# Kernel optimization log

Measured on AMD Instinct MI355X. Metric: run time of the kernel, lower is better.

## Reference

```python
import jax, jax.numpy as jnp
import numpy as np

# Circuit structure constants (match init_kwargs)
N_NODES = 32768        # number of sum nodes in this layer
N_CHILD = 65536        # number of child nodes
NNZ = 1048576          # number of sparse weight entries (avg fan-in 32)
BATCH = 128


def setup_inputs() -> dict:
    key = jax.random.key(0)
    k1, k2, k3, k4 = jax.random.split(key, 4)
    # child log-likelihoods per sample (output of child layers)
    child_ll = jax.random.normal(k1, (BATCH, N_CHILD), dtype=jnp.float32)
    # sparse log-weights of the BCOO weight matrix [N_NODES, N_CHILD]
    log_w = jax.random.normal(k2, (NNZ,), dtype=jnp.float32)
    rows = jnp.sort(jax.random.randint(k3, (NNZ,), 0, N_NODES)).astype(jnp.int64)
    cols = jax.random.randint(k4, (NNZ,), 0, N_CHILD).astype(jnp.int64)
    return {"child_ll": child_ll, "log_w": log_w, "rows": rows, "cols": cols}


def reference(child_ll, log_w, rows, cols):
    """Faithful jax translation of SumLayer.log_likelihood_of_nodes.

    Original: per sample, exponentiate BCOO log-weights and child
    log-likelihoods, sparse matvec (weights @ exp(child_ll)), then
    log(result) - log_normalization_constants, where the normalization
    constants are log(row-sums of exp(log_weights)).
    """
    w = jnp.exp(log_w)  # [NNZ]
    # log normalization constants: log of row-sums of exp(log_weights)
    log_z = jnp.log(jax.ops.segment_sum(w, rows, num_segments=N_NODES))  # [N_NODES]

    def per_sample(ll):  # ll: [N_CHILD]
        p = jnp.exp(ll)
        contrib = w * p[cols]                                   # gather + weight [NNZ]
        return jax.ops.segment_sum(contrib, rows, num_segments=N_NODES)  # [N_NODES]

    s = jax.vmap(per_sample)(child_ll)  # [BATCH, N_NODES]
    return jnp.log(s) - log_z
```

## Files before the change

kernel.cpp:

```cpp
#include <hip/hip_runtime.h>
#include <math.h>

#define BATCH     128
#define N_NODES   32768
#define N_CHILD   65536
#define NNZ_TOTAL 1048576

typedef __attribute__((ext_vector_type(2))) float fx2;

__global__ __launch_bounds__(256) void exp_transpose_fp8_kernel(
    const float* __restrict__ child_ll, unsigned char* __restrict__ ex8,
    float* __restrict__ winv) {
    __shared__ float tile[64][BATCH + 1];
    __shared__ float sc[64];
    const int c0 = blockIdx.x * 64;
    const int t  = threadIdx.x;

    {
        const int cl = t & 63;
        const int b0 = t >> 6;
#pragma unroll
        for (int j = 0; j < BATCH / 4; ++j) {
            const int b = b0 + j * 4;
            tile[cl][b] = expf(child_ll[(size_t)b * N_CHILD + c0 + cl]);
        }
    }
    __syncthreads();

    if (t < 64) {
        float m = tile[t][0];
#pragma unroll 4
        for (int b = 1; b < BATCH; ++b) m = fmaxf(m, tile[t][b]);
        const int k = 7 - ilogbf(m);
        sc[t] = ldexpf(1.f, k);
        winv[c0 + t] = ldexpf(1.f, -k);
    }
    __syncthreads();

    {
        const int sub = t & 7;
        const int b0  = sub * 16;
#pragma unroll
        for (int p = 0; p < 2; ++p) {
            const int c = (t >> 3) + p * 32;
            const float s = sc[c];
            uint4 o;
            unsigned* ow = (unsigned*)&o;
#pragma unroll
            for (int q = 0; q < 4; ++q) {
                unsigned v = 0;
                v = __builtin_amdgcn_cvt_pk_fp8_f32(
                        tile[c][b0 + q * 4 + 0] * s, tile[c][b0 + q * 4 + 1] * s, v, false);
                v = __builtin_amdgcn_cvt_pk_fp8_f32(
                        tile[c][b0 + q * 4 + 2] * s, tile[c][b0 + q * 4 + 3] * s, v, true);
                ow[q] = v;
            }
            *(uint4*)&ex8[(size_t)(c0 + c) * 128 + (unsigned)b0] = o;
        }
    }
}

__global__ __launch_bounds__(256) void prep_kernel(
    const float* __restrict__ log_w, const int* __restrict__ cols,
    const float* __restrict__ winv, const int* __restrict__ rows,
    float* __restrict__ wfold, int* __restrict__ row_start) {
    const int bid = blockIdx.x;
    const int t   = threadIdx.x;
    if (bid < 1024) {
        const int i = (bid * 256 + t) * 4;
        const float4 lw = *(const float4*)&log_w[i];
        const int4   cc = *(const int4*)&cols[i];
        float4 o;
        o.x = expf(lw.x) * winv[cc.x];
        o.y = expf(lw.y) * winv[cc.y];
        o.z = expf(lw.z) * winv[cc.z];
        o.w = expf(lw.w) * winv[cc.w];
        *(float4*)&wfold[i] = o;
    } else {
        const int r = (bid - 1024) * 256 + t;
        if (r > N_NODES) return;
        if (r == N_NODES) { row_start[r] = NNZ_TOTAL; return; }
        int lo = 0, hi = NNZ_TOTAL;
        while (lo < hi) {
            const int mid = (lo + hi) >> 1;
            if (rows[mid] < r) lo = mid + 1; else hi = mid;
        }
        row_start[r] = lo;
    }
}

__global__ __launch_bounds__(256, 4) void sum_rows_kernel(
    const unsigned char* __restrict__ ex8, const float* __restrict__ wfold,
    const float* __restrict__ log_w, const int* __restrict__ cols,
    const int* __restrict__ row_start, float* __restrict__ out) {
    const int wave = threadIdx.x >> 6;
    const int lane = threadIdx.x & 63;
    const int bid  = blockIdx.x;
    const int rb   = (bid & 7) * (N_NODES / 4 / 8) + (bid >> 3);
    const int r    = rb * 4 + wave;

    const int start = row_start[r];
    const int end   = row_start[r + 1];
    const int  slot = lane >> 3;
    const unsigned sub = (unsigned)lane & 7u;
    const unsigned boff = sub * 16u;

    float acc[16];
#pragma unroll
    for (int k = 0; k < 16; ++k) acc[k] = 0.f;
    float wlane = 0.f;

    for (int base = start; base < end; base += 64) {
        const int  idx   = base + lane;
        const bool valid = idx < end;
        const int   c  = __builtin_nontemporal_load(&cols[valid ? idx : start]);
        const float wf = valid ? __builtin_nontemporal_load(&wfold[idx]) : 0.f;
        wlane += valid ? expf(__builtin_nontemporal_load(&log_w[idx])) : 0.f;
        const int seg = end - base;

        int   ct[8];
        float wt[8];
        uint4 g[8];

#pragma unroll
        for (int t8 = 0; t8 < 8; ++t8) {
            if (t8 * 8 < seg) {
                const int pa = (t8 * 8 + slot) * 4;
                ct[t8] = __builtin_amdgcn_ds_bpermute(pa, c);
                wt[t8] = __uint_as_float(__builtin_amdgcn_ds_bpermute(
                    pa, __float_as_uint(wf)));
            }
        }
#pragma unroll
        for (int t8 = 0; t8 < 8; ++t8) {
            if (t8 * 8 < seg)
                g[t8] = *(const uint4*)(ex8 +
                        ((size_t)(unsigned)ct[t8] << 7) + boff);
        }
#pragma unroll
        for (int t8 = 0; t8 < 8; ++t8) {
            if (t8 * 8 < seg) {
                const float wtv = wt[t8];
                const unsigned* gu = (const unsigned*)&g[t8];
#pragma unroll
                for (int q = 0; q < 4; ++q) {
                    const fx2 lo = __builtin_amdgcn_cvt_pk_f32_fp8((int)gu[q], false);
                    const fx2 hi = __builtin_amdgcn_cvt_pk_f32_fp8((int)gu[q], true);
                    acc[q * 4 + 0] = fmaf(wtv, lo.x, acc[q * 4 + 0]);
                    acc[q * 4 + 1] = fmaf(wtv, lo.y, acc[q * 4 + 1]);
                    acc[q * 4 + 2] = fmaf(wtv, hi.x, acc[q * 4 + 2]);
                    acc[q * 4 + 3] = fmaf(wtv, hi.y, acc[q * 4 + 3]);
                }
            }
        }
    }

#pragma unroll
    for (int k = 0; k < 16; ++k) {
        acc[k] += __shfl_xor(acc[k], 8, 64);
        acc[k] += __shfl_xor(acc[k], 16, 64);
        acc[k] += __shfl_xor(acc[k], 32, 64);
    }
    float wsum = wlane;
#pragma unroll
    for (int m = 1; m < 64; m <<= 1) wsum += __shfl_xor(wsum, m, 64);
    const float logz = logf(wsum);

    if (lane < 8) {
        const int b0 = lane * 16;
#pragma unroll
        for (int k = 0; k < 16; ++k)
            out[(size_t)(b0 + k) * N_NODES + r] = logf(acc[k]) - logz;
    }
}

extern "C" void kernel_launch(void* const* d_in, const int* in_sizes, int n_in,
                              void* d_out, int out_size, void* d_ws, size_t ws_size,
                              hipStream_t stream) {
    const float* child_ll = (const float*)d_in[0];
    const float* log_w    = (const float*)d_in[1];
    const int*   rows     = (const int*)d_in[2];
    const int*   cols     = (const int*)d_in[3];
    float*       out      = (float*)d_out;

    unsigned char* ex8    = (unsigned char*)d_ws;
    float* winv      = (float*)((char*)d_ws + (size_t)N_CHILD * 128);
    float* wfold     = (float*)((char*)winv + (size_t)N_CHILD * 4);
    int*   row_start = (int*)((char*)wfold + (size_t)NNZ_TOTAL * 4);

    exp_transpose_fp8_kernel<<<N_CHILD / 64, 256, 0, stream>>>(child_ll, ex8, winv);
    prep_kernel<<<1024 + 129, 256, 0, stream>>>(log_w, cols, winv, rows,
                                                wfold, row_start);
    sum_rows_kernel<<<N_NODES / 4, 256, 0, stream>>>(ex8, wfold, log_w, cols,
                                                     row_start, out);
}
```

Baseline: 70.88 us.

## Restructure exp/fp8 pack, move log-normalizer to prep, LDS reduction in row kernel

The exp/transpose kernel now keeps child values in registers, picks the scale from the raw max via floor(x*log2e), folds the scale into exp2, and stages packed fp8 bytes through LDS. The prep kernel computes the per-row log normalizer with 16-lane groups next to the binary search, so the row kernel no longer reads log_w or runs exp on it. The row kernel loads cols and weights directly per slot instead of using bpermute, and replaces shuffle reductions with an LDS reduction so all 64 lanes write outputs. This trades redundant per-slot global loads and an extra barrier for less ALU work and wider stores.

```diff
diff --git a/kernel.cpp b/kernel.cpp
--- a/kernel.cpp
+++ b/kernel.cpp
@@ -5,65 +5,73 @@
 #define N_NODES   32768
 #define N_CHILD   65536
 #define NNZ_TOTAL 1048576
+#define LOG2E     1.44269504f
 
 typedef __attribute__((ext_vector_type(2))) float fx2;
 
-__global__ __launch_bounds__(256) void exp_transpose_fp8_kernel(
+__global__ __launch_bounds__(256) void exp8_kernel(
     const float* __restrict__ child_ll, unsigned char* __restrict__ ex8,
     float* __restrict__ winv) {
-    __shared__ float tile[64][BATCH + 1];
-    __shared__ float sc[64];
     const int c0 = blockIdx.x * 64;
     const int t  = threadIdx.x;
-
-    {
-        const int cl = t & 63;
-        const int b0 = t >> 6;
-#pragma unroll
-        for (int j = 0; j < BATCH / 4; ++j) {
-            const int b = b0 + j * 4;
-            tile[cl][b] = expf(child_ll[(size_t)b * N_CHILD + c0 + cl]);
-        }
-    }
-    __syncthreads();
-
+    const int cl = t & 63;
+    const int q  = t >> 6;
+
+    float v[32];
+    float m = -3.4e38f;
+    const float* bp = child_ll + (size_t)(q * 32) * N_CHILD + c0 + cl;
+#pragma unroll
+    for (int j = 0; j < 32; ++j) {
+        v[j] = bp[(size_t)j * N_CHILD];
+        m = fmaxf(m, v[j]);
+    }
+
+    __shared__ float smx[4][64];
+    __shared__ float skf[64];
+    smx[q][cl] = m;
+    __syncthreads();
     if (t < 64) {
-        float m = tile[t][0];
-#pragma unroll 4
-        for (int b = 1; b < BATCH; ++b) m = fmaxf(m, tile[t][b]);
-        const int k = 7 - ilogbf(m);
-        sc[t] = ldexpf(1.f, k);
-        winv[c0 + t] = ldexpf(1.f, -k);
-    }
-    __syncthreads();
-
-    {
-        const int sub = t & 7;
-        const int b0  = sub * 16;
-#pragma unroll
-        for (int p = 0; p < 2; ++p) {
-            const int c = (t >> 3) + p * 32;
-            const float s = sc[c];
-            uint4 o;
-            unsigned* ow = (unsigned*)&o;
-#pragma unroll
-            for (int q = 0; q < 4; ++q) {
-                unsigned v = 0;
-                v = __builtin_amdgcn_cvt_pk_fp8_f32(
-                        tile[c][b0 + q * 4 + 0] * s, tile[c][b0 + q * 4 + 1] * s, v, false);
-                v = __builtin_amdgcn_cvt_pk_fp8_f32(
-                        tile[c][b0 + q * 4 + 2] * s, tile[c][b0 + q * 4 + 3] * s, v, true);
-                ow[q] = v;
-            }
-            *(uint4*)&ex8[(size_t)(c0 + c) * 128 + (unsigned)b0] = o;
-        }
+        const float mm = fmaxf(fmaxf(smx[0][t], smx[1][t]),
+                               fmaxf(smx[2][t], smx[3][t]));
+        const int ks = 7 - (int)floorf(mm * LOG2E);
+        skf[t] = (float)ks;
+        winv[c0 + t] = exp2f((float)(-ks));
+    }
+    __syncthreads();
+    const float kf = skf[cl];
+
+    unsigned ow[8];
+#pragma unroll
+    for (int p = 0; p < 8; ++p) {
+        const float a0 = exp2f(fmaf(v[4 * p + 0], LOG2E, kf));
+        const float a1 = exp2f(fmaf(v[4 * p + 1], LOG2E, kf));
+        const float a2 = exp2f(fmaf(v[4 * p + 2], LOG2E, kf));
+        const float a3 = exp2f(fmaf(v[4 * p + 3], LOG2E, kf));
+        unsigned u = 0;
+        u = __builtin_amdgcn_cvt_pk_fp8_f32(a0, a1, u, false);
+        u = __builtin_amdgcn_cvt_pk_fp8_f32(a2, a3, u, true);
+        ow[p] = u;
+    }
+
+    __shared__ unsigned char sby[64 * 144];
+    *(uint4*)&sby[cl * 144 + q * 32]      = *(uint4*)&ow[0];
+    *(uint4*)&sby[cl * 144 + q * 32 + 16] = *(uint4*)&ow[4];
+    __syncthreads();
+
+    const int sub = t & 7, cc = t >> 3;
+#pragma unroll
+    for (int p = 0; p < 2; ++p) {
+        const int c = cc + p * 32;
+        *(uint4*)&ex8[(size_t)(c0 + c) * 128 + sub * 16] =
+            *(const uint4*)&sby[c * 144 + sub * 16];
     }
 }
 
 __global__ __launch_bounds__(256) void prep_kernel(
     const float* __restrict__ log_w, const int* __restrict__ cols,
     const float* __restrict__ winv, const int* __restrict__ rows,
-    float* __restrict__ wfold, int* __restrict__ row_start) {
+    float* __restrict__ wfold, int* __restrict__ row_start,
+    float* __restrict__ logzv) {
     const int bid = blockIdx.x;
     const int t   = threadIdx.x;
     if (bid < 1024) {
@@ -76,23 +84,37 @@
         o.z = expf(lw.z) * winv[cc.z];
         o.w = expf(lw.w) * winv[cc.w];
         *(float4*)&wfold[i] = o;
+        if (bid == 0 && t == 0) row_start[N_NODES] = NNZ_TOTAL;
     } else {
-        const int r = (bid - 1024) * 256 + t;
-        if (r > N_NODES) return;
-        if (r == N_NODES) { row_start[r] = NNZ_TOTAL; return; }
+        const int wave = t >> 6, lane = t & 63;
+        const int grp = lane >> 4, j = lane & 15;
+        const int r = (bid - 1024) * 16 + wave * 4 + grp;
         int lo = 0, hi = NNZ_TOTAL;
         while (lo < hi) {
             const int mid = (lo + hi) >> 1;
             if (rows[mid] < r) lo = mid + 1; else hi = mid;
         }
-        row_start[r] = lo;
+        const int s = lo;
+        int lo2 = s, hi2 = NNZ_TOTAL;
+        while (lo2 < hi2) {
+            const int mid = (lo2 + hi2) >> 1;
+            if (rows[mid] < r + 1) lo2 = mid + 1; else hi2 = mid;
+        }
+        const int e = lo2;
+        float sum = 0.f;
+        for (int i = s + j; i < e; i += 16) sum += expf(log_w[i]);
+        sum += __shfl_xor(sum, 1, 64);
+        sum += __shfl_xor(sum, 2, 64);
+        sum += __shfl_xor(sum, 4, 64);
+        sum += __shfl_xor(sum, 8, 64);
+        if (j == 0) { row_start[r] = s; logzv[r] = logf(sum); }
     }
 }
 
 __global__ __launch_bounds__(256, 4) void sum_rows_kernel(
     const unsigned char* __restrict__ ex8, const float* __restrict__ wfold,
-    const float* __restrict__ log_w, const int* __restrict__ cols,
-    const int* __restrict__ row_start, float* __restrict__ out) {
+    const int* __restrict__ cols, const int* __restrict__ row_start,
+    const float* __restrict__ logzv, float* __restrict__ out) {
     const int wave = threadIdx.x >> 6;
     const int lane = threadIdx.x & 63;
     const int bid  = blockIdx.x;
@@ -101,23 +123,16 @@
 
     const int start = row_start[r];
     const int end   = row_start[r + 1];
-    const int  slot = lane >> 3;
-    const unsigned sub = (unsigned)lane & 7u;
-    const unsigned boff = sub * 16u;
+    const int slot  = lane >> 3;
+    const int sub   = lane & 7;
+    const unsigned boff = (unsigned)sub * 16u;
 
     float acc[16];
 #pragma unroll
     for (int k = 0; k < 16; ++k) acc[k] = 0.f;
-    float wlane = 0.f;
 
     for (int base = start; base < end; base += 64) {
-        const int  idx   = base + lane;
-        const bool valid = idx < end;
-        const int   c  = __builtin_nontemporal_load(&cols[valid ? idx : start]);
-        const float wf = valid ? __builtin_nontemporal_load(&wfold[idx]) : 0.f;
-        wlane += valid ? expf(__builtin_nontemporal_load(&log_w[idx])) : 0.f;
         const int seg = end - base;
-
         int   ct[8];
         float wt[8];
         uint4 g[8];
@@ -125,10 +140,9 @@
 #pragma unroll
         for (int t8 = 0; t8 < 8; ++t8) {
             if (t8 * 8 < seg) {
-                const int pa = (t8 * 8 + slot) * 4;
-                ct[t8] = __builtin_amdgcn_ds_bpermute(pa, c);
-                wt[t8] = __uint_as_float(__builtin_amdgcn_ds_bpermute(
-                    pa, __float_as_uint(wf)));
+                const int i = base + t8 * 8 + slot;
+                ct[t8] = cols[min(i, NNZ_TOTAL - 1)];
+                wt[t8] = (i < end) ? wfold[i] : 0.f;
             }
         }
 #pragma unroll
@@ -155,23 +169,26 @@
         }
     }
 
-#pragma unroll
-    for (int k = 0; k < 16; ++k) {
-        acc[k] += __shfl_xor(acc[k], 8, 64);
-        acc[k] += __shfl_xor(acc[k], 16, 64);
-        acc[k] += __shfl_xor(acc[k], 32, 64);
-    }
-    float wsum = wlane;
-#pragma unroll
-    for (int m = 1; m < 64; m <<= 1) wsum += __shfl_xor(wsum, m, 64);
-    const float logz = logf(wsum);
-
-    if (lane < 8) {
-        const int b0 = lane * 16;
-#pragma unroll
-        for (int k = 0; k < 16; ++k)
-            out[(size_t)(b0 + k) * N_NODES + r] = logf(acc[k]) - logz;
-    }
+    __shared__ float red[4][8][132];
+#pragma unroll
+    for (int u = 0; u < 4; ++u) {
+        const float4 vv = {acc[4 * u], acc[4 * u + 1],
+                           acc[4 * u + 2], acc[4 * u + 3]};
+        *(float4*)&red[wave][slot][sub * 16 + 4 * u] = vv;
+    }
+    __syncthreads();
+
+    const int b0 = lane * 2;
+    float s0 = 0.f, s1 = 0.f;
+#pragma unroll
+    for (int sl = 0; sl < 8; ++sl) {
+        const float2 p = *(const float2*)&red[wave][sl][b0];
+        s0 += p.x;
+        s1 += p.y;
+    }
+    const float lz = logzv[r];
+    out[(size_t)b0 * N_NODES + r]       = logf(s0) - lz;
+    out[(size_t)(b0 + 1) * N_NODES + r] = logf(s1) - lz;
 }
 
 extern "C" void kernel_launch(void* const* d_in, const int* in_sizes, int n_in,
@@ -183,14 +200,15 @@
     const int*   cols     = (const int*)d_in[3];
     float*       out      = (float*)d_out;
 
-    unsigned char* ex8    = (unsigned char*)d_ws;
+    unsigned char* ex8 = (unsigned char*)d_ws;
     float* winv      = (float*)((char*)d_ws + (size_t)N_CHILD * 128);
     float* wfold     = (float*)((char*)winv + (size_t)N_CHILD * 4);
     int*   row_start = (int*)((char*)wfold + (size_t)NNZ_TOTAL * 4);
-
-    exp_transpose_fp8_kernel<<<N_CHILD / 64, 256, 0, stream>>>(child_ll, ex8, winv);
-    prep_kernel<<<1024 + 129, 256, 0, stream>>>(log_w, cols, winv, rows,
-                                                wfold, row_start);
-    sum_rows_kernel<<<N_NODES / 4, 256, 0, stream>>>(ex8, wfold, log_w, cols,
-                                                     row_start, out);
-}
+    float* logzv     = (float*)((char*)row_start + (size_t)(N_NODES + 1) * 4);
+
+    exp8_kernel<<<N_CHILD / 64, 256, 0, stream>>>(child_ll, ex8, winv);
+    prep_kernel<<<3072, 256, 0, stream>>>(log_w, cols, winv, rows,
+                                          wfold, row_start, logzv);
+    sum_rows_kernel<<<N_NODES / 4, 256, 0, stream>>>(ex8, wfold, cols,
+                                                     row_start, logzv, out);
+}
```

New measurement: 84.05 us. 18.6% more time.
